# Kernel tuning notes

Measured on AMD Instinct MI355X. Metric: run time of the kernel, lower is better.

## Reference

```python
import jax, jax.numpy as jnp
import numpy as np

N_SEG, B, COND = 16, 256, 512
H, OUT = 1024, 512


def setup_inputs() -> dict:
    key = jax.random.key(0)
    ks = jax.random.split(key, 14)
    s = 0.05  # keep gates in non-saturated range
    return {
        "c": jax.random.normal(ks[0], (N_SEG, B, COND), jnp.float32),
        "W_init": jax.random.normal(ks[1], (4 * H, COND), jnp.float32) * s,
        "b_init": jax.random.normal(ks[2], (4 * H,), jnp.float32) * s,
        "W_ih1": jax.random.normal(ks[3], (4 * H, COND + OUT), jnp.float32) * s,
        "W_hh1": jax.random.normal(ks[4], (4 * H, H), jnp.float32) * s,
        "b_ih1": jax.random.normal(ks[5], (4 * H,), jnp.float32) * s,
        "b_hh1": jax.random.normal(ks[6], (4 * H,), jnp.float32) * s,
        "W_ih2": jax.random.normal(ks[7], (4 * H, H), jnp.float32) * s,
        "W_hh2": jax.random.normal(ks[8], (4 * H, H), jnp.float32) * s,
        "b_ih2": jax.random.normal(ks[9], (4 * H,), jnp.float32) * s,
        "b_hh2": jax.random.normal(ks[10], (4 * H,), jnp.float32) * s,
        "W_out": jax.random.normal(ks[11], (OUT, H), jnp.float32) * s,
        "b_out": jax.random.normal(ks[12], (OUT,), jnp.float32) * s,
        "length": 32,
        "epoch": 10,
        "k": 200,
    }


def _lstm_cell(x, h, c, W_ih, W_hh, b_ih, b_hh):
    # PyTorch LSTMCell gate order: input, forget, cell, output
    g = x @ W_ih.T + b_ih + h @ W_hh.T + b_hh
    i, f, gg, o = jnp.split(g, 4, axis=-1)
    c_new = jax.nn.sigmoid(f) * c + jax.nn.sigmoid(i) * jnp.tanh(gg)
    h_new = jax.nn.sigmoid(o) * jnp.tanh(c_new)
    return h_new, c_new


def reference(c, W_init, b_init, W_ih1, W_hh1, b_ih1, b_hh1,
              W_ih2, W_hh2, b_ih2, b_hh2, W_out, b_out,
              length, epoch, k):
    steps = length // 2
    n_seg, bsz, _ = c.shape

    def segment(prev, embed):
        # fresh LSTM states from the conductor embedding
        t = jnp.tanh(embed @ W_init.T + b_init)  # [B, 4H]
        h1, h2, c1, c2 = jnp.split(t, 4, axis=-1)

        def step(carry, _):
            h1, c1, h2, c2, prev = carry
            prev = jax.lax.stop_gradient(prev)  # training=False path: detach
            x = jnp.concatenate([embed, prev], axis=1)  # [B, COND+OUT]
            h1n, c1n = _lstm_cell(x, h1, c1, W_ih1, W_hh1, b_ih1, b_hh1)
            h2n, c2n = _lstm_cell(h1n, h2, c2, W_ih2, W_hh2, b_ih2, b_hh2)
            out = h2n @ W_out.T + b_out  # [B, OUT]
            return (h1n, c1n, h2n, c2n, out), out

        (_, _, _, _, prev), outs = jax.lax.scan(
            step, (h1, h2_init := h2, c1, c2, prev)[:0] or (h1, c1, h2, c2, prev),
            None, length=steps)
        return prev, outs  # outs: [steps, B, OUT]

    prev0 = jnp.zeros((bsz, OUT), dtype=c.dtype)
    _, outs = jax.lax.scan(segment, prev0, c)  # [n_seg, steps, B, OUT]
    outputs = outs.reshape(n_seg * steps, bsz, OUT).transpose(1, 0, 2)
    ratio = jnp.float32(k / (k + np.exp(epoch / k)))
    return outputs, ratio
```

## Files before the change

kernel.cpp:

```cpp
#include <hip/hip_runtime.h>
#include <hip/hip_bf16.h>

using bf16 = __hip_bfloat16;
typedef __attribute__((ext_vector_type(8))) short bf16x8;
typedef __attribute__((ext_vector_type(4))) float f32x4;

__device__ __forceinline__ void gload16(const void* g, void* l) {
  __builtin_amdgcn_global_load_lds((const __attribute__((address_space(1))) void*)g,
                                   (__attribute__((address_space(3))) void*)l, 16, 0, 0);
}

__device__ __forceinline__ float sigm(float x) { return 1.0f / (1.0f + __expf(-x)); }
__device__ __forceinline__ float ftanh(float x) {
  float e = __expf(2.0f * fabsf(x));
  return copysignf(1.0f - 2.0f / (e + 1.0f), x);
}

#define MFMA16(a, b, c) __builtin_amdgcn_mfma_f32_16x16x32_bf16(a, b, c, 0, 0, 0)

__global__ __launch_bounds__(512) void rnn_step(
    const bf16* __restrict__ a1, const bf16* __restrict__ a2,
    const bf16* __restrict__ w1, const bf16* __restrict__ w2,
    const float* __restrict__ pe, const float* __restrict__ bias,
    const float* __restrict__ bsub,
    const float* __restrict__ c_in, float* __restrict__ c_out,
    bf16* __restrict__ h_out)
{
  __shared__ __attribute__((aligned(128))) char smem[65536];
  const int tid = threadIdx.x;
  const int wv = tid >> 6, ln = tid & 63;
  const int grp = wv >> 2, wg = wv & 3;
  const int nt = blockIdx.x, mt = blockIdx.y;
  const int m0 = mt << 6, n0 = nt << 6;
  const int wm = (wg >> 1) << 5, wn = (wg & 1) << 5;
  const bool use2 = (a2 != nullptr);

  const bf16* asrc = (grp == 0) ? a1 : (use2 ? a2 : a1);
  const bf16* wsrc = (grp == 0) ? w1 : (use2 ? w2 : w1);

  char* gbase = smem + (grp << 15);

  auto stage = [&](int kb) {
    char* As = gbase + ((kb & 1) << 14);
    char* Bs = As + 8192;
    const int k0b = kb << 7;
#pragma unroll
    for (int i = 0; i < 2; ++i) {
      int rr = ((i << 2) + wg) * 8 + (ln >> 3);
      int sc = (ln & 7) ^ (rr & 7);
      gload16((const char*)asrc + ((size_t)(m0 + rr) << 11) + k0b + (sc << 4),
              As + (((i << 2) + wg) << 10));
      gload16((const char*)wsrc + ((size_t)(n0 + rr) << 11) + k0b + (sc << 4),
              Bs + (((i << 2) + wg) << 10));
    }
  };

  f32x4 acc00{}, acc01{}, acc10{}, acc11{};

  stage(0);
  for (int kb = 0; kb < 16; ++kb) {
    asm volatile("s_waitcnt vmcnt(0)" ::: "memory");
    __builtin_amdgcn_s_barrier();
    asm volatile("" ::: "memory");
    if (kb + 1 < 16) stage(kb + 1);
    const char* As = gbase + ((kb & 1) << 14);
    const char* Bs = As + 8192;
    __builtin_amdgcn_s_setprio(1);
#pragma unroll
    for (int ks = 0; ks < 2; ++ks) {
      const int kc = (ks << 2) + (ln >> 4);
      auto ld = [&](const char* base, int row) -> bf16x8 {
        return *(const bf16x8*)(base + row * 128 + ((kc ^ (row & 7)) << 4));
      };
      bf16x8 A0 = ld(As, wm + (ln & 15));
      bf16x8 A1 = ld(As, wm + 16 + (ln & 15));
      bf16x8 B0 = ld(Bs, wn + (ln & 15));
      bf16x8 B1 = ld(Bs, wn + 16 + (ln & 15));
      acc00 = MFMA16(A0, B0, acc00);
      acc01 = MFMA16(A0, B1, acc01);
      acc10 = MFMA16(A1, B0, acc10);
      acc11 = MFMA16(A1, B1, acc11);
    }
    __builtin_amdgcn_s_setprio(0);
  }

  __syncthreads();
  float* gs = (float*)smem;
#pragma unroll
  for (int mi = 0; mi < 2; ++mi)
#pragma unroll
    for (int ni = 0; ni < 2; ++ni) {
      f32x4 a = (mi == 0) ? (ni == 0 ? acc00 : acc01) : (ni == 0 ? acc10 : acc11);
#pragma unroll
      for (int r = 0; r < 4; ++r) {
        int row = wm + mi * 16 + ((ln >> 4) << 2) + r;
        int col = wn + ni * 16 + (ln & 15);
        gs[grp * 4352 + row * 68 + col] = a[r];
      }
    }
  __syncthreads();

  const int h  = tid & 15;
  const int mr = tid >> 4;
  const int hg = (nt << 4) + h;
#pragma unroll
  for (int half = 0; half < 2; ++half) {
    int m  = mr + (half << 5);
    int gm = m0 + m;
    float4 v = *(const float4*)(gs + m * 68 + (h << 2));
    float g0 = v.x, g1 = v.y, g2 = v.z, g3 = v.w;
    if (use2) {
      float4 u = *(const float4*)(gs + 4352 + m * 68 + (h << 2));
      g0 += u.x; g1 += u.y; g2 += u.z; g3 += u.w;
    }
    int nb = n0 + (h << 2);
    if (pe) {
      float4 pv = *(const float4*)(pe + (size_t)gm * 4096 + nb);
      g0 += pv.x; g1 += pv.y; g2 += pv.z; g3 += pv.w;
    }
    if (bias) {
      float4 bv = *(const float4*)(bias + nb);
      g0 += bv.x; g1 += bv.y; g2 += bv.z; g3 += bv.w;
    }
    if (bsub) {
      float4 sv = *(const float4*)(bsub + nb);
      g0 -= sv.x; g1 -= sv.y; g2 -= sv.z; g3 -= sv.w;
    }
    float ig = sigm(g0), fg = sigm(g1), gg = ftanh(g2), og = sigm(g3);
    size_t idx = (size_t)gm * 1024 + hg;
    float cn = fg * c_in[idx] + ig * gg;
    c_out[idx] = cn;
    h_out[idx] = __float2bfloat16(og * ftanh(cn));
  }
}

template <int EP>
__global__ __launch_bounds__(256) void gemm_ep(
    const bf16* __restrict__ A, const bf16* __restrict__ W, int K,
    const float* __restrict__ bias,
    float* __restrict__ f1, float* __restrict__ f2,
    bf16* __restrict__ o1, bf16* __restrict__ o2, int gt_base)
{
  __shared__ __attribute__((aligned(128))) char smem[32768];
  const int tid = threadIdx.x;
  const int wv = tid >> 6, ln = tid & 63;
  const int n0 = blockIdx.x << 6;
  const int m0 = blockIdx.y << 6;
  const int Nn = (int)(gridDim.x << 6);
  const int wm = (wv >> 1) << 5, wn = (wv & 1) << 5;
  const int nkb = K >> 6;

  f32x4 acc00{}, acc01{}, acc10{}, acc11{};

  auto stage = [&](int kb, int buf) {
    int k0 = kb << 6;
    char* As = smem + buf * 16384;
    char* Bs = As + 8192;
#pragma unroll
    for (int i = 0; i < 2; ++i) {
      int r  = ((i << 2) + wv) * 8 + (ln >> 3);
      int sc = (ln & 7) ^ (r & 7);
      gload16((const char*)(A + (size_t)(m0 + r) * K + k0) + (sc << 4),
              As + (((i << 2) + wv) << 10));
      gload16((const char*)(W + (size_t)(n0 + r) * K + k0) + (sc << 4),
              Bs + (((i << 2) + wv) << 10));
    }
  };

  stage(0, 0);
  __syncthreads();
  for (int kb = 0; kb < nkb; ++kb) {
    int buf = kb & 1;
    if (kb + 1 < nkb) stage(kb + 1, buf ^ 1);
    const char* As = smem + buf * 16384;
    const char* Bs = As + 8192;
#pragma unroll
    for (int ks = 0; ks < 2; ++ks) {
      const int kc = (ks << 2) + (ln >> 4);
      auto ld = [&](const char* base, int row) -> bf16x8 {
        return *(const bf16x8*)(base + row * 128 + ((kc ^ (row & 7)) << 4));
      };
      bf16x8 A0 = ld(As, wm + (ln & 15));
      bf16x8 A1 = ld(As, wm + 16 + (ln & 15));
      bf16x8 B0 = ld(Bs, wn + (ln & 15));
      bf16x8 B1 = ld(Bs, wn + 16 + (ln & 15));
      acc00 = MFMA16(A0, B0, acc00);
      acc01 = MFMA16(A0, B1, acc01);
      acc10 = MFMA16(A1, B0, acc10);
      acc11 = MFMA16(A1, B1, acc11);
    }
    __syncthreads();
  }

#pragma unroll
  for (int mi = 0; mi < 2; ++mi)
#pragma unroll
    for (int ni = 0; ni < 2; ++ni) {
      f32x4 a = (mi == 0) ? (ni == 0 ? acc00 : acc01) : (ni == 0 ? acc10 : acc11);
#pragma unroll
      for (int r = 0; r < 4; ++r) {
        int m = m0 + wm + mi * 16 + ((ln >> 4) << 2) + r;
        int n = n0 + wn + ni * 16 + (ln & 15);
        float v = a[r];
        if constexpr (EP == 0) {
          o1[(size_t)m * Nn + n] = __float2bfloat16(v);
        } else if constexpr (EP == 1) {
          v = tanhf(v + bias[n]);
          int q = n >> 10, hh = n & 1023;
          size_t idx = (size_t)m * 1024 + hh;
          if (q == 0)      o1[idx] = __float2bfloat16(v);
          else if (q == 1) o2[idx] = __float2bfloat16(v);
          else if (q == 2) f1[idx] = v;
          else             f2[idx] = v;
        } else if constexpr (EP == 2) {
          f1[(size_t)m * 4096 + n] = v + bias[n];
        } else {
          int b = m & 255, g = (m >> 8) + gt_base;
          f1[(size_t)b * 131072 + (size_t)g * 512 + n] = v + bias[n];
        }
      }
    }
}

__global__ void k_conv(const float* __restrict__ s, bf16* __restrict__ d, int n) {
  int i = blockIdx.x * 256 + threadIdx.x;
  if (i < n) d[i] = __float2bfloat16(s[i]);
}
__global__ void k_trans_wout(const float* __restrict__ s, bf16* __restrict__ d) {
  int i = blockIdx.x * 256 + threadIdx.x;
  int l = i >> 9, j = i & 511;
  d[i] = __float2bfloat16(s[(size_t)j * 1024 + l]);
}
__global__ void k_reorder_g(const float* __restrict__ s, bf16* __restrict__ d) {
  int i = blockIdx.x * 256 + threadIdx.x;
  int np = i >> 10, kx = i & 1023;
  int hh = np >> 2, q = np & 3;
  d[i] = __float2bfloat16(s[(size_t)(q * 1024 + hh) * 1024 + kx]);
}
__global__ void k_reorder_c(const float* __restrict__ s, bf16* __restrict__ d, int coloff) {
  int i = blockIdx.x * 256 + threadIdx.x;
  int np = i >> 9, kx = i & 511;
  int hh = np >> 2, q = np & 3;
  d[i] = __float2bfloat16(s[(size_t)(q * 1024 + hh) * 1024 + coloff + kx]);
}
__global__ void k_bias(const float* __restrict__ bih1, const float* __restrict__ bhh1,
                       const float* __restrict__ bih2, const float* __restrict__ bhh2,
                       const float* __restrict__ bo,   const float* __restrict__ Wih1,
                       float* __restrict__ b1r, float* __restrict__ b2r,
                       float* __restrict__ bfr) {
  int n = blockIdx.x * 256 + threadIdx.x;
  int hh = n >> 2, q = n & 3, r = q * 1024 + hh;
  const float* wrow = Wih1 + (size_t)r * 1024 + 512;
  float acc = 0.f;
  for (int j = 0; j < 512; ++j) acc += bo[j] * wrow[j];
  bfr[n] = acc;
  b1r[n] = bih1[r] + bhh1[r] + acc;
  b2r[n] = bih2[r] + bhh2[r];
}
__global__ void k_ratio(float* __restrict__ dst, const int* __restrict__ ep,
                        const int* __restrict__ kv) {
  float kf = (float)kv[0];
  dst[0] = kf / (kf + __expf((float)ep[0] / kf));
}

extern "C" void kernel_launch(void* const* d_in, const int* in_sizes, int n_in,
                              void* d_out, int out_size, void* d_ws, size_t ws_size,
                              hipStream_t stream) {
  (void)in_sizes; (void)n_in;
  const float* in_c     = (const float*)d_in[0];
  const float* in_Winit = (const float*)d_in[1];
  const float* in_binit = (const float*)d_in[2];
  const float* in_Wih1  = (const float*)d_in[3];
  const float* in_Whh1  = (const float*)d_in[4];
  const float* in_bih1  = (const float*)d_in[5];
  const float* in_bhh1  = (const float*)d_in[6];
  const float* in_Wih2  = (const float*)d_in[7];
  const float* in_Whh2  = (const float*)d_in[8];
  const float* in_bih2  = (const float*)d_in[9];
  const float* in_bhh2  = (const float*)d_in[10];
  const float* in_Wout  = (const float*)d_in[11];
  const float* in_bout  = (const float*)d_in[12];
  const int*   in_epoch = (const int*)d_in[14];
  const int*   in_k     = (const int*)d_in[15];
  float* out = (float*)d_out;

  char* p = (char*)d_ws;
  auto alloc = [&](size_t bytes) { char* q = p; p += (bytes + 255) & ~(size_t)255; return q; };
  bf16* wHH1  = (bf16*)alloc(4096ull * 1024 * 2);
  bf16* wFOLD = (bf16*)alloc(4096ull * 1024 * 2);
  bf16* wIH2  = (bf16*)alloc(4096ull * 1024 * 2);
  bf16* wHH2  = (bf16*)alloc(4096ull * 1024 * 2);
  bf16* wOUT  = (bf16*)alloc(512ull * 1024 * 2);
  bf16* wOUTT = (bf16*)alloc(1024ull * 512 * 2);
  bf16* wINIT = (bf16*)alloc(4096ull * 512 * 2);
  bf16* wIH1C = (bf16*)alloc(4096ull * 512 * 2);
  bf16* wPREV = (bf16*)alloc(4096ull * 512 * 2);
  bf16* cbf   = (bf16*)alloc(4096ull * 512 * 2);
  float* b1r  = (float*)alloc(4096 * 4);
  float* b2r  = (float*)alloc(4096 * 4);
  float* bfr  = (float*)alloc(4096 * 4);
  bf16* h1i   = (bf16*)alloc(16ull * 256 * 1024 * 2);
  bf16* h2i   = (bf16*)alloc(16ull * 256 * 1024 * 2);
  float* c1i  = (float*)alloc(16ull * 256 * 1024 * 4);
  float* c2i  = (float*)alloc(16ull * 256 * 1024 * 4);
  float* PE1  = (float*)alloc(16ull * 256 * 4096 * 4);
  bf16* h1b[2]; float* c1b[2]; float* c2b[2]; bf16* h2b[2];
  for (int i = 0; i < 2; ++i) {
    h1b[i] = (bf16*)alloc(256ull * 1024 * 2);
    c1b[i] = (float*)alloc(256ull * 1024 * 4);
    c2b[i] = (float*)alloc(256ull * 1024 * 4);
    h2b[i] = (bf16*)alloc(256ull * 1024 * 2);
  }
  bf16* hist = (bf16*)alloc(256ull * 256 * 1024 * 2);
  size_t need_hist = (size_t)(p - (char*)d_ws);
  bool primary = ws_size >= need_hist;

  k_conv<<<8192, 256, 0, stream>>>(in_c, cbf, 2097152);
  k_conv<<<2048, 256, 0, stream>>>(in_Wout, wOUT, 524288);
  k_conv<<<8192, 256, 0, stream>>>(in_Winit, wINIT, 2097152);
  k_trans_wout<<<2048, 256, 0, stream>>>(in_Wout, wOUTT);
  k_reorder_g<<<16384, 256, 0, stream>>>(in_Whh1, wHH1);
  k_reorder_g<<<16384, 256, 0, stream>>>(in_Wih2, wIH2);
  k_reorder_g<<<16384, 256, 0, stream>>>(in_Whh2, wHH2);
  k_reorder_c<<<8192, 256, 0, stream>>>(in_Wih1, wIH1C, 0);
  k_reorder_c<<<8192, 256, 0, stream>>>(in_Wih1, wPREV, 512);
  k_bias<<<16, 256, 0, stream>>>(in_bih1, in_bhh1, in_bih2, in_bhh2, in_bout,
                                 in_Wih1, b1r, b2r, bfr);
  gemm_ep<0><<<dim3(16, 64), 256, 0, stream>>>(wPREV, wOUTT, 512, nullptr,
                                               nullptr, nullptr, wFOLD, nullptr, 0);
  gemm_ep<1><<<dim3(64, 64), 256, 0, stream>>>(cbf, wINIT, 512, in_binit,
                                               c1i, c2i, h1i, h2i, 0);
  gemm_ep<2><<<dim3(64, 64), 256, 0, stream>>>(cbf, wIH1C, 512, b1r,
                                               PE1, nullptr, nullptr, nullptr, 0);

  const size_t S = 256ull * 1024;
  for (int s = 0; s < 16; ++s) {
    for (int t = 0; t < 16; ++t) {
      int gt = s * 16 + t;
      int cur = gt & 1, prv = cur ^ 1;
      const bf16* h2prev = (gt == 0) ? nullptr
                          : (primary ? hist + (size_t)(gt - 1) * S : h2b[prv]);
      rnn_step<<<dim3(64, 4), 512, 0, stream>>>(
          (t == 0) ? h1i + (size_t)s * S : h1b[prv], h2prev,
          wHH1, wFOLD,
          PE1 + (size_t)s * 1048576, nullptr, (gt == 0) ? bfr : nullptr,
          (t == 0) ? c1i + (size_t)s * S : c1b[prv], c1b[cur], h1b[cur]);
      rnn_step<<<dim3(64, 4), 512, 0, stream>>>(
          h1b[cur],
          (t == 0) ? h2i + (size_t)s * S
                   : (primary ? hist + (size_t)(gt - 1) * S : h2b[prv]),
          wIH2, wHH2, nullptr, b2r, nullptr,
          (t == 0) ? c2i + (size_t)s * S : c2b[prv], c2b[cur],
          primary ? hist + (size_t)gt * S : h2b[cur]);
      if (!primary) {
        gemm_ep<3><<<dim3(8, 4), 256, 0, stream>>>(h2b[cur], wOUT, 1024, in_bout,
                                                   out, nullptr, nullptr, nullptr, gt);
      }
    }
  }

  if (primary) {
    gemm_ep<3><<<dim3(8, 1024), 256, 0, stream>>>(hist, wOUT, 1024, in_bout,
                                                  out, nullptr, nullptr, nullptr, 0);
  }
  k_ratio<<<1, 1, 0, stream>>>(out + (out_size - 1), in_epoch, in_k);
}
```

Baseline: 7.041 ms.

## Replace per-step LSTM launches with one persistent kernel using grid barriers

Swaps 512 per-timestep kernel launches for a single persistent kernel of 256 workgroups that loops over all 256 timesteps. Workgroups sync through an atomic global barrier, keep cell states in registers, and prefetch the next GEMM's weight and independent activation tiles before each barrier. The aim is to remove launch overhead and global c-state traffic. The design assumes all 256 blocks are co-resident, which one block per CU on MI355X appears to allow. A spin barrier costs latency and risks deadlock if blocks are not all resident.

```diff
diff --git a/kernel.cpp b/kernel.cpp
--- a/kernel.cpp
+++ b/kernel.cpp
@@ -17,6 +17,191 @@
 }
 
 #define MFMA16(a, b, c) __builtin_amdgcn_mfma_f32_16x16x32_bf16(a, b, c, 0, 0, 0)
+
+#define RD 16
+
+__global__ __launch_bounds__(512) void rnn_persist(
+    const bf16* __restrict__ wHH1, const bf16* __restrict__ wFOLD,
+    const bf16* __restrict__ wIH2, const bf16* __restrict__ wHH2,
+    const float* __restrict__ PE1, const float* __restrict__ b2r,
+    const float* __restrict__ bfr,
+    const bf16* __restrict__ h1i, const bf16* __restrict__ h2i,
+    const float* __restrict__ c1i, const float* __restrict__ c2i,
+    bf16* __restrict__ h1ring, bf16* __restrict__ hist,
+    unsigned* __restrict__ bar)
+{
+  const size_t S = 256ull * 1024;
+  const int tid = threadIdx.x;
+  const int wv = tid >> 6, ln = tid & 63, grp = wv >> 2, wg = wv & 3;
+  const int xcd = blockIdx.x & 7, slot = blockIdx.x >> 3;
+  const int nt = (xcd << 3) | (slot & 7), mt = slot >> 3;
+  const int m0 = mt << 6, n0 = nt << 6;
+  const int wm = (wg >> 1) << 5, wn = (wg & 1) << 5;
+
+  __shared__ __attribute__((aligned(128))) char smem[65536];
+  char* gbase = smem + (grp << 15);
+
+  const int eh = tid & 15, emr = tid >> 4;
+  const int ehg = (nt << 4) + eh;
+
+  f32x4 acc00, acc01, acc10, acc11;
+  float c1r[2], c2r[2];
+  unsigned ep = 0;
+
+  auto stageA = [&](int kb, const bf16* asrc) {
+    char* As = gbase + ((kb & 1) << 14);
+    const int k0b = kb << 7;
+#pragma unroll
+    for (int i = 0; i < 2; ++i) {
+      int rr = ((i << 2) + wg) * 8 + (ln >> 3);
+      int sc = (ln & 7) ^ (rr & 7);
+      gload16((const char*)asrc + ((size_t)(m0 + rr) << 11) + k0b + (sc << 4),
+              As + (((i << 2) + wg) << 10));
+    }
+  };
+  auto stageB = [&](int kb, const bf16* wsrc) {
+    char* Bs = gbase + ((kb & 1) << 14) + 8192;
+    const int k0b = kb << 7;
+#pragma unroll
+    for (int i = 0; i < 2; ++i) {
+      int rr = ((i << 2) + wg) * 8 + (ln >> 3);
+      int sc = (ln & 7) ^ (rr & 7);
+      gload16((const char*)wsrc + ((size_t)(n0 + rr) << 11) + k0b + (sc << 4),
+              Bs + (((i << 2) + wg) << 10));
+    }
+  };
+
+  auto gemm = [&](const bf16* asrc, const bf16* wsrc) {
+    acc00 = f32x4{0.f, 0.f, 0.f, 0.f}; acc01 = acc00; acc10 = acc00; acc11 = acc00;
+    for (int kb = 0; kb < 16; ++kb) {
+      asm volatile("s_waitcnt vmcnt(0)" ::: "memory");
+      __builtin_amdgcn_s_barrier();
+      asm volatile("" ::: "memory");
+      if (kb + 1 < 16) { stageA(kb + 1, asrc); stageB(kb + 1, wsrc); }
+      const char* As = gbase + ((kb & 1) << 14);
+      const char* Bs = As + 8192;
+      __builtin_amdgcn_s_setprio(1);
+#pragma unroll
+      for (int ks = 0; ks < 2; ++ks) {
+        const int kc = (ks << 2) + (ln >> 4);
+        auto ld = [&](const char* base, int row) -> bf16x8 {
+          return *(const bf16x8*)(base + row * 128 + ((kc ^ (row & 7)) << 4));
+        };
+        bf16x8 A0 = ld(As, wm + (ln & 15));
+        bf16x8 A1 = ld(As, wm + 16 + (ln & 15));
+        bf16x8 B0 = ld(Bs, wn + (ln & 15));
+        bf16x8 B1 = ld(Bs, wn + 16 + (ln & 15));
+        acc00 = MFMA16(A0, B0, acc00);
+        acc01 = MFMA16(A0, B1, acc01);
+        acc10 = MFMA16(A1, B0, acc10);
+        acc11 = MFMA16(A1, B1, acc11);
+      }
+      __builtin_amdgcn_s_setprio(0);
+    }
+  };
+
+  auto epilogue = [&](bool dual, const float* pe, const float* bias, const float* bsub,
+                      bool loadc, const float* ci, float* creg, bf16* hout) {
+    __syncthreads();
+    float* gs = (float*)smem;
+#pragma unroll
+    for (int mi = 0; mi < 2; ++mi)
+#pragma unroll
+      for (int ni = 0; ni < 2; ++ni) {
+        f32x4 a = (mi == 0) ? (ni == 0 ? acc00 : acc01) : (ni == 0 ? acc10 : acc11);
+#pragma unroll
+        for (int r = 0; r < 4; ++r) {
+          int row = wm + mi * 16 + ((ln >> 4) << 2) + r;
+          int col = wn + ni * 16 + (ln & 15);
+          gs[grp * 4352 + row * 68 + col] = a[r];
+        }
+      }
+    __syncthreads();
+#pragma unroll
+    for (int half = 0; half < 2; ++half) {
+      int m = emr + (half << 5);
+      int gm = m0 + m;
+      float4 v = *(const float4*)(gs + m * 68 + (eh << 2));
+      float g0 = v.x, g1 = v.y, g2 = v.z, g3 = v.w;
+      if (dual) {
+        float4 u = *(const float4*)(gs + 4352 + m * 68 + (eh << 2));
+        g0 += u.x; g1 += u.y; g2 += u.z; g3 += u.w;
+      }
+      int nb = n0 + (eh << 2);
+      if (pe) {
+        float4 pv = *(const float4*)(pe + (size_t)gm * 4096 + nb);
+        g0 += pv.x; g1 += pv.y; g2 += pv.z; g3 += pv.w;
+      }
+      if (bias) {
+        float4 bv = *(const float4*)(bias + nb);
+        g0 += bv.x; g1 += bv.y; g2 += bv.z; g3 += bv.w;
+      }
+      if (bsub) {
+        float4 sv = *(const float4*)(bsub + nb);
+        g0 -= sv.x; g1 -= sv.y; g2 -= sv.z; g3 -= sv.w;
+      }
+      float ig = sigm(g0), fg = sigm(g1), gg = ftanh(g2), og = sigm(g3);
+      size_t idx = (size_t)gm * 1024 + ehg;
+      float cc = loadc ? ci[idx] : creg[half];
+      float cn = fg * cc + ig * gg;
+      creg[half] = cn;
+      hout[idx] = __float2bfloat16(og * ftanh(cn));
+    }
+    __syncthreads();
+  };
+
+  auto gbar = [&]() {
+    __syncthreads();
+    if (tid == 0) {
+      __builtin_amdgcn_fence(__ATOMIC_RELEASE, "agent");
+      unsigned arr = __hip_atomic_fetch_add(bar, 1u, __ATOMIC_RELAXED,
+                                            __HIP_MEMORY_SCOPE_AGENT);
+      if (arr == ep * 256u + 255u) {
+        __hip_atomic_store(bar + 32, ep + 1u, __ATOMIC_RELAXED,
+                           __HIP_MEMORY_SCOPE_AGENT);
+      } else {
+        while (__hip_atomic_load(bar + 32, __ATOMIC_RELAXED,
+                                 __HIP_MEMORY_SCOPE_AGENT) <= ep)
+          __builtin_amdgcn_s_sleep(2);
+      }
+    }
+    __syncthreads();
+    asm volatile("" ::: "memory");
+    ep++;
+  };
+
+  stageB(0, grp ? wFOLD : wHH1);
+  stageA(0, h1i);
+
+  for (int gt = 0; gt < 256; ++gt) {
+    const int s = gt >> 4, t = gt & 15;
+    const bf16* A1 = (t == 0) ? h1i + (size_t)s * S
+                              : h1ring + (size_t)((gt - 1) & (RD - 1)) * S;
+    const bf16* A2 = (gt == 0) ? A1 : hist + (size_t)(gt - 1) * S;
+    const bf16* sa = grp ? A2 : A1;
+    gemm(sa, grp ? wFOLD : wHH1);
+    epilogue(gt != 0, PE1 + (size_t)s * 1048576, nullptr, (gt == 0) ? bfr : nullptr,
+             t == 0, c1i + (size_t)s * S, c1r,
+             h1ring + (size_t)(gt & (RD - 1)) * S);
+    const bf16* l2a2 = (t == 0) ? h2i + (size_t)s * S : hist + (size_t)(gt - 1) * S;
+    stageB(0, grp ? wHH2 : wIH2);
+    if (grp == 1) stageA(0, l2a2);
+    gbar();
+    const bf16* l2a1 = h1ring + (size_t)(gt & (RD - 1)) * S;
+    if (grp == 0) stageA(0, l2a1);
+    gemm(grp ? l2a2 : l2a1, grp ? wHH2 : wIH2);
+    epilogue(true, nullptr, b2r, nullptr, t == 0, c2i + (size_t)s * S, c2r,
+             hist + (size_t)gt * S);
+    int gn = (gt + 1 < 256) ? gt + 1 : gt;
+    int s2 = gn >> 4, t2 = gn & 15;
+    const bf16* n1a = (t2 == 0) ? h1i + (size_t)s2 * S
+                                : h1ring + (size_t)(gt & (RD - 1)) * S;
+    stageB(0, grp ? wFOLD : wHH1);
+    if (grp == 0) stageA(0, n1a);
+    gbar();
+    if (grp == 1) stageA(0, hist + (size_t)gt * S);
+  }
+}
 
 __global__ __launch_bounds__(512) void rnn_step(
     const bf16* __restrict__ a1, const bf16* __restrict__ a2,
@@ -37,7 +222,6 @@
 
   const bf16* asrc = (grp == 0) ? a1 : (use2 ? a2 : a1);
   const bf16* wsrc = (grp == 0) ? w1 : (use2 ? w2 : w1);
-
   char* gbase = smem + (grp << 15);
 
   auto stage = [&](int kb) {
@@ -56,7 +240,6 @@
   };
 
   f32x4 acc00{}, acc01{}, acc10{}, acc11{};
-
   stage(0);
   for (int kb = 0; kb < 16; ++kb) {
     asm volatile("s_waitcnt vmcnt(0)" ::: "memory");
@@ -100,12 +283,11 @@
     }
   __syncthreads();
 
-  const int h  = tid & 15;
-  const int mr = tid >> 4;
+  const int h = tid & 15, mr = tid >> 4;
   const int hg = (nt << 4) + h;
 #pragma unroll
   for (int half = 0; half < 2; ++half) {
-    int m  = mr + (half << 5);
+    int m = mr + (half << 5);
     int gm = m0 + m;
     float4 v = *(const float4*)(gs + m * 68 + (h << 2));
     float g0 = v.x, g1 = v.y, g2 = v.z, g3 = v.w;
@@ -114,18 +296,12 @@
       g0 += u.x; g1 += u.y; g2 += u.z; g3 += u.w;
     }
     int nb = n0 + (h << 2);
-    if (pe) {
-      float4 pv = *(const float4*)(pe + (size_t)gm * 4096 + nb);
-      g0 += pv.x; g1 += pv.y; g2 += pv.z; g3 += pv.w;
-    }
-    if (bias) {
-      float4 bv = *(const float4*)(bias + nb);
-      g0 += bv.x; g1 += bv.y; g2 += bv.z; g3 += bv.w;
-    }
-    if (bsub) {
-      float4 sv = *(const float4*)(bsub + nb);
-      g0 -= sv.x; g1 -= sv.y; g2 -= sv.z; g3 -= sv.w;
-    }
+    if (pe) { float4 pv = *(const float4*)(pe + (size_t)gm * 4096 + nb);
+              g0 += pv.x; g1 += pv.y; g2 += pv.z; g3 += pv.w; }
+    if (bias){ float4 bv = *(const float4*)(bias + nb);
+              g0 += bv.x; g1 += bv.y; g2 += bv.z; g3 += bv.w; }
+    if (bsub){ float4 sv = *(const float4*)(bsub + nb);
+              g0 -= sv.x; g1 -= sv.y; g2 -= sv.z; g3 -= sv.w; }
     float ig = sigm(g0), fg = sigm(g1), gg = ftanh(g2), og = sigm(g3);
     size_t idx = (size_t)gm * 1024 + hg;
     float cn = fg * c_in[idx] + ig * gg;
@@ -158,7 +334,7 @@
     char* Bs = As + 8192;
 #pragma unroll
     for (int i = 0; i < 2; ++i) {
-      int r  = ((i << 2) + wv) * 8 + (ln >> 3);
+      int r = ((i << 2) + wv) * 8 + (ln >> 3);
       int sc = (ln & 7) ^ (r & 7);
       gload16((const char*)(A + (size_t)(m0 + r) * K + k0) + (sc << 4),
               As + (((i << 2) + wv) << 10));
@@ -262,6 +438,9 @@
   float kf = (float)kv[0];
   dst[0] = kf / (kf + __expf((float)ep[0] / kf));
 }
+__global__ void k_zero(unsigned* __restrict__ p) {
+  if (threadIdx.x < 64) p[threadIdx.x] = 0u;
+}
 
 extern "C" void kernel_launch(void* const* d_in, const int* in_sizes, int n_in,
                               void* d_out, int out_size, void* d_ws, size_t ws_size,
@@ -299,6 +478,7 @@
   float* b1r  = (float*)alloc(4096 * 4);
   float* b2r  = (float*)alloc(4096 * 4);
   float* bfr  = (float*)alloc(4096 * 4);
+  unsigned* bar = (unsigned*)alloc(4096);
   bf16* h1i   = (bf16*)alloc(16ull * 256 * 1024 * 2);
   bf16* h2i   = (bf16*)alloc(16ull * 256 * 1024 * 2);
   float* c1i  = (float*)alloc(16ull * 256 * 1024 * 4);
@@ -311,9 +491,13 @@
     c2b[i] = (float*)alloc(256ull * 1024 * 4);
     h2b[i] = (bf16*)alloc(256ull * 1024 * 2);
   }
+  bf16* h1ring = (bf16*)alloc((size_t)RD * 256 * 1024 * 2);
+  size_t need_nohist = (size_t)(p - (char*)d_ws);
   bf16* hist = (bf16*)alloc(256ull * 256 * 1024 * 2);
-  size_t need_hist = (size_t)(p - (char*)d_ws);
-  bool primary = ws_size >= need_hist;
+  size_t need_full = (size_t)(p - (char*)d_ws);
+  bool persist = ws_size >= need_full;
+  bool primary = ws_size >= need_full;
+  (void)need_nohist;
 
   k_conv<<<8192, 256, 0, stream>>>(in_c, cbf, 2097152);
   k_conv<<<2048, 256, 0, stream>>>(in_Wout, wOUT, 524288);
@@ -326,6 +510,7 @@
   k_reorder_c<<<8192, 256, 0, stream>>>(in_Wih1, wPREV, 512);
   k_bias<<<16, 256, 0, stream>>>(in_bih1, in_bhh1, in_bih2, in_bhh2, in_bout,
                                  in_Wih1, b1r, b2r, bfr);
+  k_zero<<<1, 64, 0, stream>>>(bar);
   gemm_ep<0><<<dim3(16, 64), 256, 0, stream>>>(wPREV, wOUTT, 512, nullptr,
                                                nullptr, nullptr, wFOLD, nullptr, 0);
   gemm_ep<1><<<dim3(64, 64), 256, 0, stream>>>(cbf, wINIT, 512, in_binit,
@@ -334,34 +519,40 @@
                                                PE1, nullptr, nullptr, nullptr, 0);
 
   const size_t S = 256ull * 1024;
-  for (int s = 0; s < 16; ++s) {
-    for (int t = 0; t < 16; ++t) {
-      int gt = s * 16 + t;
-      int cur = gt & 1, prv = cur ^ 1;
-      const bf16* h2prev = (gt == 0) ? nullptr
-                          : (primary ? hist + (size_t)(gt - 1) * S : h2b[prv]);
-      rnn_step<<<dim3(64, 4), 512, 0, stream>>>(
-          (t == 0) ? h1i + (size_t)s * S : h1b[prv], h2prev,
-          wHH1, wFOLD,
-          PE1 + (size_t)s * 1048576, nullptr, (gt == 0) ? bfr : nullptr,
-          (t == 0) ? c1i + (size_t)s * S : c1b[prv], c1b[cur], h1b[cur]);
-      rnn_step<<<dim3(64, 4), 512, 0, stream>>>(
-          h1b[cur],
-          (t == 0) ? h2i + (size_t)s * S
-                   : (primary ? hist + (size_t)(gt - 1) * S : h2b[prv]),
-          wIH2, wHH2, nullptr, b2r, nullptr,
-          (t == 0) ? c2i + (size_t)s * S : c2b[prv], c2b[cur],
-          primary ? hist + (size_t)gt * S : h2b[cur]);
-      if (!primary) {
-        gemm_ep<3><<<dim3(8, 4), 256, 0, stream>>>(h2b[cur], wOUT, 1024, in_bout,
-                                                   out, nullptr, nullptr, nullptr, gt);
-      }
-    }
-  }
-
-  if (primary) {
+  if (persist) {
+    rnn_persist<<<256, 512, 0, stream>>>(wHH1, wFOLD, wIH2, wHH2, PE1, b2r, bfr,
+                                         h1i, h2i, c1i, c2i, h1ring, hist, bar);
     gemm_ep<3><<<dim3(8, 1024), 256, 0, stream>>>(hist, wOUT, 1024, in_bout,
                                                   out, nullptr, nullptr, nullptr, 0);
+  } else {
+    for (int s = 0; s < 16; ++s) {
+      for (int t = 0; t < 16; ++t) {
+        int gt = s * 16 + t;
+        int cur = gt & 1, prv = cur ^ 1;
+        const bf16* h2prev = (gt == 0) ? nullptr
+                            : (primary ? hist + (size_t)(gt - 1) * S : h2b[prv]);
+        rnn_step<<<dim3(64, 4), 512, 0, stream>>>(
+            (t == 0) ? h1i + (size_t)s * S : h1b[prv], h2prev,
+            wHH1, wFOLD,
+            PE1 + (size_t)s * 1048576, nullptr, (gt == 0) ? bfr : nullptr,
+            (t == 0) ? c1i + (size_t)s * S : c1b[prv], c1b[cur], h1b[cur]);
+        rnn_step<<<dim3(64, 4), 512, 0, stream>>>(
+            h1b[cur],
+            (t == 0) ? h2i + (size_t)s * S
+                     : (primary ? hist + (size_t)(gt - 1) * S : h2b[prv]),
+            wIH2, wHH2, nullptr, b2r, nullptr,
+            (t == 0) ? c2i + (size_t)s * S : c2b[prv], c2b[cur],
+            primary ? hist + (size_t)gt * S : h2b[cur]);
+        if (!primary) {
+          gemm_ep<3><<<dim3(8, 4), 256, 0, stream>>>(h2b[cur], wOUT, 1024, in_bout,
+                                                     out, nullptr, nullptr, nullptr, gt);
+        }
+      }
+    }
+    if (primary) {
+      gemm_ep<3><<<dim3(8, 1024), 256, 0, stream>>>(hist, wOUT, 1024, in_bout,
+                                                    out, nullptr, nullptr, nullptr, 0);
+    }
   }
   k_ratio<<<1, 1, 0, stream>>>(out + (out_size - 1), in_epoch, in_k);
 }
```

Result: slower. 7.880 ms (+11.9%).

## Deepen rnn_step K-pipeline to 4 stages with register double-buffered fragments and swizzled grid

Applied to the files above, without the earlier changes.

The rnn_step GEMM loop now stages 64-byte K chunks into a 4-deep LDS ring instead of 128-byte chunks double-buffered. It waits with vmcnt(2) so two loads stay in flight, and it prefetches the next MFMA fragments into registers while the current ones compute. Block indices are remapped from a 1D grid so that consecutive blocks spread across the N tiles, which may change L2 reuse of the weights. The aim is to hide global load latency in the per-timestep recurrent GEMMs, at the cost of twice as many barriers per K and a new LDS swizzle.

```diff
diff --git a/kernel.cpp b/kernel.cpp
--- a/kernel.cpp
+++ b/kernel.cpp
@@ -17,6 +17,11 @@
 }
 
 #define MFMA16(a, b, c) __builtin_amdgcn_mfma_f32_16x16x32_bf16(a, b, c, 0, 0, 0)
+#define WAITV2() asm volatile("s_waitcnt vmcnt(2)" ::: "memory")
+#define WAITV0() asm volatile("s_waitcnt vmcnt(0)" ::: "memory")
+#define BARRIER() do { __builtin_amdgcn_s_barrier(); asm volatile("" ::: "memory"); } while (0)
+
+struct Frag { bf16x8 a0, a1, b0, b1; };
 
 __global__ __launch_bounds__(512) void rnn_step(
     const bf16* __restrict__ a1, const bf16* __restrict__ a2,
@@ -30,59 +35,73 @@
   const int tid = threadIdx.x;
   const int wv = tid >> 6, ln = tid & 63;
   const int grp = wv >> 2, wg = wv & 3;
-  const int nt = blockIdx.x, mt = blockIdx.y;
+  const int bid = blockIdx.x;
+  const int nt = ((bid & 7) << 3) | ((bid >> 3) & 7);
+  const int mt = bid >> 6;
   const int m0 = mt << 6, n0 = nt << 6;
   const int wm = (wg >> 1) << 5, wn = (wg & 1) << 5;
   const bool use2 = (a2 != nullptr);
 
   const bf16* asrc = (grp == 0) ? a1 : (use2 ? a2 : a1);
   const bf16* wsrc = (grp == 0) ? w1 : (use2 ? w2 : w1);
-
   char* gbase = smem + (grp << 15);
 
+  const int srow = (wg << 4) + (ln >> 2);
+  const int skc  = (ln & 3) ^ ((srow >> 1) & 3);
+  const size_t aGOff = ((size_t)(m0 + srow) << 11) + (skc << 4);
+  const size_t bGOff = ((size_t)(n0 + srow) << 11) + (skc << 4);
+
   auto stage = [&](int kb) {
-    char* As = gbase + ((kb & 1) << 14);
-    char* Bs = As + 8192;
-    const int k0b = kb << 7;
-#pragma unroll
-    for (int i = 0; i < 2; ++i) {
-      int rr = ((i << 2) + wg) * 8 + (ln >> 3);
-      int sc = (ln & 7) ^ (rr & 7);
-      gload16((const char*)asrc + ((size_t)(m0 + rr) << 11) + k0b + (sc << 4),
-              As + (((i << 2) + wg) << 10));
-      gload16((const char*)wsrc + ((size_t)(n0 + rr) << 11) + k0b + (sc << 4),
-              Bs + (((i << 2) + wg) << 10));
-    }
+    char* dst = gbase + ((kb & 3) << 13) + (wg << 10);
+    gload16((const char*)asrc + aGOff + ((size_t)kb << 6), dst);
+    gload16((const char*)wsrc + bGOff + ((size_t)kb << 6), dst + 4096);
   };
 
+  const int kc = ln >> 4;
+  const int ar0 = wm + (ln & 15), ar1 = ar0 + 16;
+  const int br0 = wn + (ln & 15), br1 = br0 + 16;
+  const int aoff0 = ar0 * 64 + ((kc ^ ((ar0 >> 1) & 3)) << 4);
+  const int aoff1 = ar1 * 64 + ((kc ^ ((ar1 >> 1) & 3)) << 4);
+  const int boff0 = 4096 + br0 * 64 + ((kc ^ ((br0 >> 1) & 3)) << 4);
+  const int boff1 = 4096 + br1 * 64 + ((kc ^ ((br1 >> 1) & 3)) << 4);
+
+  auto ldfrags = [&](int kb, Frag& f) {
+    const char* base = gbase + ((kb & 3) << 13);
+    f.a0 = *(const bf16x8*)(base + aoff0);
+    f.a1 = *(const bf16x8*)(base + aoff1);
+    f.b0 = *(const bf16x8*)(base + boff0);
+    f.b1 = *(const bf16x8*)(base + boff1);
+  };
+
   f32x4 acc00{}, acc01{}, acc10{}, acc11{};
-
-  stage(0);
-  for (int kb = 0; kb < 16; ++kb) {
-    asm volatile("s_waitcnt vmcnt(0)" ::: "memory");
-    __builtin_amdgcn_s_barrier();
-    asm volatile("" ::: "memory");
-    if (kb + 1 < 16) stage(kb + 1);
-    const char* As = gbase + ((kb & 1) << 14);
-    const char* Bs = As + 8192;
-    __builtin_amdgcn_s_setprio(1);
-#pragma unroll
-    for (int ks = 0; ks < 2; ++ks) {
-      const int kc = (ks << 2) + (ln >> 4);
-      auto ld = [&](const char* base, int row) -> bf16x8 {
-        return *(const bf16x8*)(base + row * 128 + ((kc ^ (row & 7)) << 4));
-      };
-      bf16x8 A0 = ld(As, wm + (ln & 15));
-      bf16x8 A1 = ld(As, wm + 16 + (ln & 15));
-      bf16x8 B0 = ld(Bs, wn + (ln & 15));
-      bf16x8 B1 = ld(Bs, wn + 16 + (ln & 15));
-      acc00 = MFMA16(A0, B0, acc00);
-      acc01 = MFMA16(A0, B1, acc01);
-      acc10 = MFMA16(A1, B0, acc10);
-      acc11 = MFMA16(A1, B1, acc11);
-    }
-    __builtin_amdgcn_s_setprio(0);
-  }
+  auto domfma = [&](Frag& f) {
+    acc00 = MFMA16(f.a0, f.b0, acc00);
+    acc01 = MFMA16(f.a0, f.b1, acc01);
+    acc10 = MFMA16(f.a1, f.b0, acc10);
+    acc11 = MFMA16(f.a1, f.b1, acc11);
+  };
+
+  Frag f0, f1;
+  stage(0); stage(1);
+  WAITV2(); BARRIER();
+  stage(2);
+  ldfrags(0, f0);
+  __builtin_amdgcn_s_setprio(1);
+  for (int kb = 1; kb < 31; kb += 2) {
+    WAITV2(); BARRIER();
+    stage(kb + 2);
+    ldfrags(kb, f1);
+    domfma(f0);
+    WAITV2(); BARRIER();
+    if (kb + 3 < 32) stage(kb + 3);
+    ldfrags(kb + 1, f0);
+    domfma(f1);
+  }
+  WAITV0(); BARRIER();
+  ldfrags(31, f1);
+  domfma(f0);
+  domfma(f1);
+  __builtin_amdgcn_s_setprio(0);
 
   __syncthreads();
   float* gs = (float*)smem;
@@ -100,12 +119,11 @@
     }
   __syncthreads();
 
-  const int h  = tid & 15;
-  const int mr = tid >> 4;
+  const int h = tid & 15, mr = tid >> 4;
   const int hg = (nt << 4) + h;
 #pragma unroll
   for (int half = 0; half < 2; ++half) {
-    int m  = mr + (half << 5);
+    int m = mr + (half << 5);
     int gm = m0 + m;
     float4 v = *(const float4*)(gs + m * 68 + (h << 2));
     float g0 = v.x, g1 = v.y, g2 = v.z, g3 = v.w;
@@ -114,18 +132,12 @@
       g0 += u.x; g1 += u.y; g2 += u.z; g3 += u.w;
     }
     int nb = n0 + (h << 2);
-    if (pe) {
-      float4 pv = *(const float4*)(pe + (size_t)gm * 4096 + nb);
-      g0 += pv.x; g1 += pv.y; g2 += pv.z; g3 += pv.w;
-    }
-    if (bias) {
-      float4 bv = *(const float4*)(bias + nb);
-      g0 += bv.x; g1 += bv.y; g2 += bv.z; g3 += bv.w;
-    }
-    if (bsub) {
-      float4 sv = *(const float4*)(bsub + nb);
-      g0 -= sv.x; g1 -= sv.y; g2 -= sv.z; g3 -= sv.w;
-    }
+    if (pe) { float4 pv = *(const float4*)(pe + (size_t)gm * 4096 + nb);
+              g0 += pv.x; g1 += pv.y; g2 += pv.z; g3 += pv.w; }
+    if (bias){ float4 bv = *(const float4*)(bias + nb);
+              g0 += bv.x; g1 += bv.y; g2 += bv.z; g3 += bv.w; }
+    if (bsub){ float4 sv = *(const float4*)(bsub + nb);
+              g0 -= sv.x; g1 -= sv.y; g2 -= sv.z; g3 -= sv.w; }
     float ig = sigm(g0), fg = sigm(g1), gg = ftanh(g2), og = sigm(g3);
     size_t idx = (size_t)gm * 1024 + hg;
     float cn = fg * c_in[idx] + ig * gg;
@@ -158,7 +170,7 @@
     char* Bs = As + 8192;
 #pragma unroll
     for (int i = 0; i < 2; ++i) {
-      int r  = ((i << 2) + wv) * 8 + (ln >> 3);
+      int r = ((i << 2) + wv) * 8 + (ln >> 3);
       int sc = (ln & 7) ^ (r & 7);
       gload16((const char*)(A + (size_t)(m0 + r) * K + k0) + (sc << 4),
               As + (((i << 2) + wv) << 10));
@@ -312,8 +324,8 @@
     h2b[i] = (bf16*)alloc(256ull * 1024 * 2);
   }
   bf16* hist = (bf16*)alloc(256ull * 256 * 1024 * 2);
-  size_t need_hist = (size_t)(p - (char*)d_ws);
-  bool primary = ws_size >= need_hist;
+  size_t need_full = (size_t)(p - (char*)d_ws);
+  bool primary = ws_size >= need_full;
 
   k_conv<<<8192, 256, 0, stream>>>(in_c, cbf, 2097152);
   k_conv<<<2048, 256, 0, stream>>>(in_Wout, wOUT, 524288);
@@ -340,12 +352,12 @@
       int cur = gt & 1, prv = cur ^ 1;
       const bf16* h2prev = (gt == 0) ? nullptr
                           : (primary ? hist + (size_t)(gt - 1) * S : h2b[prv]);
-      rnn_step<<<dim3(64, 4), 512, 0, stream>>>(
+      rnn_step<<<256, 512, 0, stream>>>(
           (t == 0) ? h1i + (size_t)s * S : h1b[prv], h2prev,
           wHH1, wFOLD,
           PE1 + (size_t)s * 1048576, nullptr, (gt == 0) ? bfr : nullptr,
           (t == 0) ? c1i + (size_t)s * S : c1b[prv], c1b[cur], h1b[cur]);
-      rnn_step<<<dim3(64, 4), 512, 0, stream>>>(
+      rnn_step<<<256, 512, 0, stream>>>(
           h1b[cur],
           (t == 0) ? h2i + (size_t)s * S
                    : (primary ? hist + (size_t)(gt - 1) * S : h2b[prv]),
```

Measured after the change: 6.608 ms. 1.07x faster.
